# Performance work log

Measured on AMD Instinct MI355X. Metric: run time of the kernel, lower is better.

Reference implementation:

```python
import jax, jax.numpy as jnp
import numpy as np

B, S, D = 4, 1024, 2048
H, G = 16, 2            # num_heads, num_groups (GQA)
HD = D // H             # head_dim = 128


def rotate_half(x):
    x1, x2 = x[..., : x.shape[-1] // 2], x[..., x.shape[-1] // 2 :]
    return jnp.concatenate([-x2, x1], axis=-1)


def setup_inputs() -> dict:
    key = jax.random.key(0)
    ks = jax.random.split(key, 9)
    scale = 0.02
    return {
        "x": jax.random.normal(ks[0], (B, S, D), jnp.float32),
        "wq": jax.random.normal(ks[1], (D, D), jnp.float32) * scale,
        "bq": jnp.zeros((D,), jnp.float32),
        "wk": jax.random.normal(ks[2], (D, G * HD), jnp.float32) * scale,
        "bk": jnp.zeros((G * HD,), jnp.float32),
        "wv": jax.random.normal(ks[3], (D, G * HD), jnp.float32) * scale,
        "bv": jnp.zeros((G * HD,), jnp.float32),
        "wo": jax.random.normal(ks[4], (D, D), jnp.float32) * scale,
        "bo": jnp.zeros((D,), jnp.float32),
    }


def reference(x, wq, bq, wk, bk, wv, bv, wo, bo):
    b, s, d = x.shape
    hd = HD
    # projections (flax Linear: y = x @ kernel + bias)
    q = (x @ wq + bq).reshape(b, s, H, hd)
    k = (x @ wk + bk).reshape(b, s, G, hd)
    v = (x @ wv + bv).reshape(b, s, G, hd)

    # RoPE tables (positions = arange(s), matching q_pos/kv_pos defaults)
    inv_freq = 1.0 / 10000 ** (jnp.arange(0, hd, 2, dtype=jnp.float32) / hd)
    t = jnp.arange(s, dtype=jnp.float32)
    freqs = jnp.outer(t, inv_freq)              # [s, hd/2]
    freqs = jnp.concatenate([freqs, freqs], -1)  # [s, hd]
    sin = jnp.sin(freqs)[:, None, :]             # [s, 1, hd]
    cos = jnp.cos(freqs)[:, None, :]

    q = q * cos + rotate_half(q) * sin
    q = q * (hd ** -0.5)  # module's explicit scale
    k = k * cos + rotate_half(k) * sin

    # GQA: expand K/V groups to full heads (repeats = H // G)
    reps = H // G
    k_exp = jnp.repeat(k, reps, axis=2)  # [b, s, H, hd]
    v_exp = jnp.repeat(v, reps, axis=2)

    # jax.nn.dot_product_attention also applies 1/sqrt(hd) by default,
    # so net scaling is hd**-1 (faithful to the original module).
    scores = jnp.einsum("bqhd,bkhd->bhqk", q, k_exp) * (hd ** -0.5)
    attn = jax.nn.softmax(scores, axis=-1)
    out = jnp.einsum("bhqk,bkhd->bqhd", attn, v_exp).reshape(b, s, d)
    return out @ wo + bo
```

## Files before the change

kernel.cpp:

```cpp
#include <hip/hip_runtime.h>
#include <hip/hip_bf16.h>
#include <type_traits>

typedef __attribute__((ext_vector_type(8))) __bf16 bf16x8;
typedef __attribute__((ext_vector_type(4))) float floatx4;

__device__ inline floatx4 mfma_bf16(bf16x8 a, bf16x8 b, floatx4 c) {
    return __builtin_amdgcn_mfma_f32_16x16x32_bf16(a, b, c, 0, 0, 0);
}

__device__ inline void g2l16(const __hip_bfloat16* g, __hip_bfloat16* l) {
    __builtin_amdgcn_global_load_lds(
        (const __attribute__((address_space(1))) void*)g,
        (__attribute__((address_space(3))) void*)l, 16, 0, 0);
}

__global__ void cast_f32_bf16_k(const float* __restrict__ in,
                                __hip_bfloat16* __restrict__ out, int n4) {
    int i = blockIdx.x * blockDim.x + threadIdx.x;
    if (i < n4) {
        float4 v = ((const float4*)in)[i];
        ushort4 u;
        __hip_bfloat16 a0 = __float2bfloat16(v.x), a1 = __float2bfloat16(v.y);
        __hip_bfloat16 a2 = __float2bfloat16(v.z), a3 = __float2bfloat16(v.w);
        u.x = *(unsigned short*)&a0; u.y = *(unsigned short*)&a1;
        u.z = *(unsigned short*)&a2; u.w = *(unsigned short*)&a3;
        ((ushort4*)out)[i] = u;
    }
}

__global__ void prep_k(const float* __restrict__ wq, const float* __restrict__ wk,
                       const float* __restrict__ wv, const float* __restrict__ wo,
                       const float* __restrict__ bq, const float* __restrict__ bk,
                       const float* __restrict__ bv,
                       __hip_bfloat16* __restrict__ wqkvt,
                       __hip_bfloat16* __restrict__ wot,
                       float* __restrict__ bqkv) {
    int bid = blockIdx.x;
    if (bid >= 9216) {
        int i = (bid - 9216) * 256 + threadIdx.x;
        if (i < 2560)
            bqkv[i] = (i < 2048) ? bq[i] : (i < 2304 ? bk[i - 2048] : bv[i - 2304]);
        return;
    }
    const float* W; __hip_bfloat16* Wt; int C, row_off, cb, rb;
    if (bid < 4096)      { W = wq; Wt = wqkvt; C = 2048; row_off = 0;
                           cb = bid & 63; rb = bid >> 6; }
    else if (bid < 4608) { W = wk; Wt = wqkvt; C = 256;  row_off = 2048;
                           int id = bid - 4096; cb = id & 7; rb = id >> 3; }
    else if (bid < 5120) { W = wv; Wt = wqkvt; C = 256;  row_off = 2304;
                           int id = bid - 4608; cb = id & 7; rb = id >> 3; }
    else                 { W = wo; Wt = wot;   C = 2048; row_off = 0;
                           int id = bid - 5120; cb = id & 63; rb = id >> 6; }
    __shared__ float tile[32][33];
    int c0 = cb * 32, r0 = rb * 32;
    int tx = threadIdx.x & 31, ty0 = threadIdx.x >> 5;
#pragma unroll
    for (int i = 0; i < 4; i++) {
        int ty = ty0 + i * 8;
        tile[ty][tx] = W[(size_t)(r0 + ty) * C + c0 + tx];
    }
    __syncthreads();
#pragma unroll
    for (int i = 0; i < 4; i++) {
        int ty = ty0 + i * 8;
        Wt[(size_t)(row_off + c0 + ty) * 2048 + r0 + tx] = __float2bfloat16(tile[tx][ty]);
    }
}

__global__ __launch_bounds__(256) void gemm_qkv_k(
    const __hip_bfloat16* __restrict__ A,
    const __hip_bfloat16* __restrict__ Bt,
    const float* __restrict__ bias,
    __hip_bfloat16* __restrict__ Qb,
    __hip_bfloat16* __restrict__ Kb,
    __hip_bfloat16* __restrict__ Vlin) {
    __shared__ alignas(16) __hip_bfloat16 As[128 * 32];
    __shared__ alignas(16) __hip_bfloat16 Bs[128 * 32];
    const int t = threadIdx.x, lane = t & 63, w = t >> 6;
    const int quad = lane >> 4, l16 = lane & 15;
    const int bm = blockIdx.y, bn = blockIdx.x;
    const int r_ = t >> 2;
    const int kc_ = (t & 3) ^ ((t >> 3) & 3);
    const int swz = (l16 >> 1) & 3;

    const __hip_bfloat16* gA = A + (size_t)(bm * 128 + r_) * 2048 + kc_ * 8;
    const __hip_bfloat16* gB = Bt + (size_t)(bn * 128 + r_) * 2048 + kc_ * 8;

    floatx4 acc[2][8] = {};

    for (int kt = 0; kt < 2048; kt += 32) {
        g2l16(gA + kt, As + t * 8);
        g2l16(gA + kt + 64 * 2048, As + (t + 256) * 8);
        g2l16(gB + kt, Bs + t * 8);
        g2l16(gB + kt + 64 * 2048, Bs + (t + 256) * 8);
        __syncthreads();
        bf16x8 af[2], bfr[8];
#pragma unroll
        for (int mi = 0; mi < 2; mi++)
            af[mi] = *(const bf16x8*)(As + (w * 32 + mi * 16 + l16) * 32 + (quad ^ swz) * 8);
#pragma unroll
        for (int ni = 0; ni < 8; ni++)
            bfr[ni] = *(const bf16x8*)(Bs + (ni * 16 + l16) * 32 + (quad ^ swz) * 8);
#pragma unroll
        for (int mi = 0; mi < 2; mi++)
#pragma unroll
            for (int ni = 0; ni < 8; ni++)
                acc[mi][ni] = mfma_bf16(af[mi], bfr[ni], acc[mi][ni]);
        __syncthreads();
    }

    const int row_base = bm * 128 + w * 32 + quad * 4;
    if (bn < 18) {
        const float scale = (bn < 16) ? 0.0078125f : 1.0f;
        __hip_bfloat16* dst = (bn < 16) ? Qb : Kb;
        const int nh = (bn < 16) ? 16 : 2;
        const int hh = (bn < 16) ? bn : (bn - 16);
#pragma unroll
        for (int ni = 0; ni < 4; ni++) {
            int j = ni * 16 + l16;
            float invf = __expf(-(float)j * (9.210340371976184f / 64.f));
            float bj  = bias[bn * 128 + j];
            float bj2 = bias[bn * 128 + j + 64];
#pragma unroll
            for (int mi = 0; mi < 2; mi++)
#pragma unroll
                for (int r = 0; r < 4; r++) {
                    int row = row_base + mi * 16 + r;
                    int b = row >> 10, s = row & 1023;
                    float vj  = acc[mi][ni][r] + bj;
                    float vj2 = acc[mi][ni + 4][r] + bj2;
                    float sn, cs;
                    __sincosf((float)s * invf, &sn, &cs);
                    __hip_bfloat16* op = dst + ((size_t)(b * nh + hh) * 1024 + s) * 128;
                    op[j]      = __float2bfloat16((vj * cs - vj2 * sn) * scale);
                    op[j + 64] = __float2bfloat16((vj2 * cs + vj * sn) * scale);
                }
        }
    } else {
        int g = bn - 18;
#pragma unroll
        for (int ni = 0; ni < 8; ni++) {
            int col = ni * 16 + l16;
            float bv = bias[bn * 128 + col];
#pragma unroll
            for (int mi = 0; mi < 2; mi++)
#pragma unroll
                for (int r = 0; r < 4; r++) {
                    int row = row_base + mi * 16 + r;
                    Vlin[(size_t)row * 256 + g * 128 + col] =
                        __float2bfloat16(acc[mi][ni][r] + bv);
                }
        }
    }
}

template <typename OUT_T>
__global__ __launch_bounds__(256) void gemm_bt_k(
    const __hip_bfloat16* __restrict__ A,
    const __hip_bfloat16* __restrict__ Bt,
    const float* __restrict__ bias,
    OUT_T* __restrict__ C,
    int M, int N, int K) {
    __shared__ alignas(16) __hip_bfloat16 As[128 * 32];
    __shared__ alignas(16) __hip_bfloat16 Bs[128 * 32];
    const int t = threadIdx.x;
    const int lane = t & 63;
    const int w = t >> 6;
    const int wm = w & 1, wn = w >> 1;
    const int quad = lane >> 4, l16 = lane & 15;
    const int bm = blockIdx.y, bn = blockIdx.x;
    const int r_ = t >> 2;
    const int kc_ = (t & 3) ^ ((t >> 3) & 3);
    const int swz = (l16 >> 1) & 3;

    const __hip_bfloat16* gA = A + (size_t)(bm * 128 + r_) * K + kc_ * 8;
    const __hip_bfloat16* gB = Bt + (size_t)(bn * 128 + r_) * K + kc_ * 8;

    floatx4 acc[4][4] = {};

    for (int kt = 0; kt < K; kt += 32) {
        g2l16(gA + kt, As + t * 8);
        g2l16(gA + kt + (size_t)64 * K, As + (t + 256) * 8);
        g2l16(gB + kt, Bs + t * 8);
        g2l16(gB + kt + (size_t)64 * K, Bs + (t + 256) * 8);
        __syncthreads();
        bf16x8 af[4], bfr[4];
#pragma unroll
        for (int mi = 0; mi < 4; mi++)
            af[mi] = *(const bf16x8*)(As + (wm * 64 + mi * 16 + l16) * 32 + (quad ^ swz) * 8);
#pragma unroll
        for (int ni = 0; ni < 4; ni++)
            bfr[ni] = *(const bf16x8*)(Bs + (wn * 64 + ni * 16 + l16) * 32 + (quad ^ swz) * 8);
#pragma unroll
        for (int mi = 0; mi < 4; mi++)
#pragma unroll
            for (int ni = 0; ni < 4; ni++)
                acc[mi][ni] = mfma_bf16(af[mi], bfr[ni], acc[mi][ni]);
        __syncthreads();
    }

#pragma unroll
    for (int mi = 0; mi < 4; mi++) {
        int row0 = bm * 128 + wm * 64 + mi * 16 + quad * 4;
#pragma unroll
        for (int ni = 0; ni < 4; ni++) {
            int col = bn * 128 + wn * 64 + ni * 16 + l16;
            float bv = bias[col];
#pragma unroll
            for (int r = 0; r < 4; r++) {
                float v = acc[mi][ni][r] + bv;
                if constexpr (std::is_same<OUT_T, float>::value)
                    C[(size_t)(row0 + r) * N + col] = v;
                else
                    C[(size_t)(row0 + r) * N + col] = __float2bfloat16(v);
            }
        }
    }
}

__global__ void transpose_v_k(const __hip_bfloat16* __restrict__ Vlin,
                              __hip_bfloat16* __restrict__ VT) {
    __shared__ __hip_bfloat16 tile[32][33];
    int bg = blockIdx.z;
    int b = bg >> 1, g = bg & 1;
    int s0 = blockIdx.y * 32, d0 = blockIdx.x * 32;
    int tx = threadIdx.x & 31, ty0 = threadIdx.x >> 5;
#pragma unroll
    for (int i = 0; i < 4; i++) {
        int ty = ty0 + i * 8;
        tile[ty][tx] = Vlin[(size_t)(b * 1024 + s0 + ty) * 256 + g * 128 + d0 + tx];
    }
    __syncthreads();
#pragma unroll
    for (int i = 0; i < 4; i++) {
        int ty = ty0 + i * 8;
        VT[((size_t)(b * 2 + g) * 128 + d0 + ty) * 1024 + s0 + tx] = tile[tx][ty];
    }
}

__global__ __launch_bounds__(256, 2) void attn_k(
    const __hip_bfloat16* __restrict__ Qb,
    const __hip_bfloat16* __restrict__ Kb,
    const __hip_bfloat16* __restrict__ VT,
    __hip_bfloat16* __restrict__ AO) {
    constexpr int PLD = 72;
    __shared__ alignas(16) __hip_bfloat16 Ks[64 * 128];
    __shared__ alignas(16) __hip_bfloat16 Vs[128 * 64];
    __shared__ alignas(16) __hip_bfloat16 Ps[4][32 * PLD];

    const int bh = blockIdx.x;
    const int b = bh >> 4, h = bh & 15, g = h >> 3;
    const int t = threadIdx.x, lane = t & 63, w = t >> 6;
    const int quad = lane >> 4, l16 = lane & 15;
    const int q0 = blockIdx.y * 128 + w * 32;

    const __hip_bfloat16* Qp = Qb + ((size_t)bh * 1024 + q0 + l16) * 128 + quad * 8;
    bf16x8 aq[2][4];
#pragma unroll
    for (int mi = 0; mi < 2; mi++)
#pragma unroll
        for (int kc = 0; kc < 4; kc++)
            aq[mi][kc] = *(const bf16x8*)(Qp + mi * 16 * 128 + kc * 32);

    const int bg = b * 2 + g;
    const __hip_bfloat16* Kstage = Kb + (size_t)bg * 1024 * 128
        + (t >> 4) * 128 + ((t & 15) ^ (t >> 4)) * 8;
    const __hip_bfloat16* Vstage = VT + (size_t)bg * 128 * 1024
        + (t >> 3) * 1024 + ((t & 7) ^ ((t >> 3) & 7)) * 8;

    float l_part[2][4] = {};
    floatx4 o[2][8] = {};

    for (int kv = 0; kv < 1024; kv += 64) {
#pragma unroll
        for (int j = 0; j < 4; j++)
            g2l16(Kstage + (size_t)(kv + j * 16) * 128, Ks + (j * 256 + t) * 8);
#pragma unroll
        for (int j = 0; j < 4; j++)
            g2l16(Vstage + (size_t)j * 32 * 1024 + kv, Vs + (j * 256 + t) * 8);
        __syncthreads();

        floatx4 s[2][4] = {};
#pragma unroll
        for (int nj = 0; nj < 4; nj++)
#pragma unroll
            for (int kc = 0; kc < 4; kc++) {
                bf16x8 kb = *(const bf16x8*)(Ks + (nj * 16 + l16) * 128
                                             + (((kc * 4 + quad) ^ l16) * 8));
                s[0][nj] = mfma_bf16(aq[0][kc], kb, s[0][nj]);
                s[1][nj] = mfma_bf16(aq[1][kc], kb, s[1][nj]);
            }

        __hip_bfloat16* pl = Ps[w];
#pragma unroll
        for (int mi = 0; mi < 2; mi++)
#pragma unroll
            for (int nj = 0; nj < 4; nj++)
#pragma unroll
                for (int r = 0; r < 4; r++) {
                    float p = __expf(s[mi][nj][r]);
                    l_part[mi][r] += p;
                    pl[(mi * 16 + quad * 4 + r) * PLD + nj * 16 + l16] =
                        __float2bfloat16(p);
                }
        asm volatile("s_waitcnt lgkmcnt(0)" ::: "memory");

        bf16x8 ap[2][2];
#pragma unroll
        for (int mi = 0; mi < 2; mi++)
#pragma unroll
            for (int kc2 = 0; kc2 < 2; kc2++)
                ap[mi][kc2] = *(const bf16x8*)(pl + (mi * 16 + l16) * PLD
                                               + kc2 * 32 + quad * 8);

#pragma unroll
        for (int ni = 0; ni < 8; ni++)
#pragma unroll
            for (int kc2 = 0; kc2 < 2; kc2++) {
                bf16x8 vb = *(const bf16x8*)(Vs + (ni * 16 + l16) * 64
                                             + (((kc2 * 4 + quad) ^ (l16 & 7)) * 8));
                o[0][ni] = mfma_bf16(ap[0][kc2], vb, o[0][ni]);
                o[1][ni] = mfma_bf16(ap[1][kc2], vb, o[1][ni]);
            }
        __syncthreads();
    }

#pragma unroll
    for (int mi = 0; mi < 2; mi++)
#pragma unroll
        for (int r = 0; r < 4; r++) {
            float sum = l_part[mi][r];
            sum += __shfl_xor(sum, 1);
            sum += __shfl_xor(sum, 2);
            sum += __shfl_xor(sum, 4);
            sum += __shfl_xor(sum, 8);
            float inv = 1.f / sum;
            size_t srow = (size_t)b * 1024 + q0 + mi * 16 + quad * 4 + r;
#pragma unroll
            for (int ni = 0; ni < 8; ni++)
                AO[srow * 2048 + h * 128 + ni * 16 + l16] =
                    __float2bfloat16(o[mi][ni][r] * inv);
        }
}

extern "C" void kernel_launch(void* const* d_in, const int* in_sizes, int n_in,
                              void* d_out, int out_size, void* d_ws, size_t ws_size,
                              hipStream_t stream) {
    (void)in_sizes; (void)n_in; (void)out_size; (void)ws_size;
    const float* x  = (const float*)d_in[0];
    const float* wq = (const float*)d_in[1];
    const float* bq = (const float*)d_in[2];
    const float* wk = (const float*)d_in[3];
    const float* bk = (const float*)d_in[4];
    const float* wv = (const float*)d_in[5];
    const float* bv = (const float*)d_in[6];
    const float* wo = (const float*)d_in[7];
    const float* bo = (const float*)d_in[8];
    float* out = (float*)d_out;

    char* ws = (char*)d_ws;
    __hip_bfloat16* xb    = (__hip_bfloat16*)(ws + 0);
    __hip_bfloat16* AO    = xb;
    __hip_bfloat16* wqkvt = (__hip_bfloat16*)(ws + 16777216);
    __hip_bfloat16* wot   = (__hip_bfloat16*)(ws + 27262976);
    __hip_bfloat16* Qb    = (__hip_bfloat16*)(ws + 35651584);
    __hip_bfloat16* Kb    = (__hip_bfloat16*)(ws + 52428800);
    __hip_bfloat16* Vlin  = (__hip_bfloat16*)(ws + 54525952);
    __hip_bfloat16* VT    = (__hip_bfloat16*)(ws + 56623104);
    float*          bqkv  = (float*)(ws + 58720256);

    cast_f32_bf16_k<<<8192, 256, 0, stream>>>(x, xb, 2097152);
    prep_k<<<9226, 256, 0, stream>>>(wq, wk, wv, wo, bq, bk, bv, wqkvt, wot, bqkv);
    gemm_qkv_k<<<dim3(20, 32), 256, 0, stream>>>(xb, wqkvt, bqkv, Qb, Kb, Vlin);
    transpose_v_k<<<dim3(4, 32, 8), 256, 0, stream>>>(Vlin, VT);
    attn_k<<<dim3(64, 8), 256, 0, stream>>>(Qb, Kb, VT, AO);
    gemm_bt_k<float><<<dim3(16, 32), 256, 0, stream>>>(AO, wot, bo, out, 4096, 2048, 2048);
}
```

Baseline: 281.4 us.

## Merge cast into prep kernel and double GEMM K-tile to 64 with XOR swizzle

Measured after the change: 287.1 us. +2.0%, slower.

```diff
diff --git a/kernel.cpp b/kernel.cpp
--- a/kernel.cpp
+++ b/kernel.cpp
@@ -15,43 +15,45 @@
         (__attribute__((address_space(3))) void*)l, 16, 0, 0);
 }
 
-__global__ void cast_f32_bf16_k(const float* __restrict__ in,
-                                __hip_bfloat16* __restrict__ out, int n4) {
-    int i = blockIdx.x * blockDim.x + threadIdx.x;
-    if (i < n4) {
-        float4 v = ((const float4*)in)[i];
+__global__ void prep_k(const float* __restrict__ x,
+                       const float* __restrict__ wq, const float* __restrict__ wk,
+                       const float* __restrict__ wv, const float* __restrict__ wo,
+                       const float* __restrict__ bq, const float* __restrict__ bk,
+                       const float* __restrict__ bv,
+                       __hip_bfloat16* __restrict__ xb,
+                       __hip_bfloat16* __restrict__ wqkvt,
+                       __hip_bfloat16* __restrict__ wot,
+                       float* __restrict__ bqkv) {
+    int bid = blockIdx.x;
+    if (bid < 8192) {
+        int i = bid * 256 + threadIdx.x;
+        float4 v = ((const float4*)x)[i];
         ushort4 u;
         __hip_bfloat16 a0 = __float2bfloat16(v.x), a1 = __float2bfloat16(v.y);
         __hip_bfloat16 a2 = __float2bfloat16(v.z), a3 = __float2bfloat16(v.w);
         u.x = *(unsigned short*)&a0; u.y = *(unsigned short*)&a1;
         u.z = *(unsigned short*)&a2; u.w = *(unsigned short*)&a3;
-        ((ushort4*)out)[i] = u;
-    }
-}
-
-__global__ void prep_k(const float* __restrict__ wq, const float* __restrict__ wk,
-                       const float* __restrict__ wv, const float* __restrict__ wo,
-                       const float* __restrict__ bq, const float* __restrict__ bk,
-                       const float* __restrict__ bv,
-                       __hip_bfloat16* __restrict__ wqkvt,
-                       __hip_bfloat16* __restrict__ wot,
-                       float* __restrict__ bqkv) {
-    int bid = blockIdx.x;
-    if (bid >= 9216) {
-        int i = (bid - 9216) * 256 + threadIdx.x;
-        if (i < 2560)
-            bqkv[i] = (i < 2048) ? bq[i] : (i < 2304 ? bk[i - 2048] : bv[i - 2304]);
+        ((ushort4*)xb)[i] = u;
         return;
     }
+    if (bid >= 17408) {
+#pragma unroll
+        for (int it = 0; it < 10; it++) {
+            int i = it * 256 + threadIdx.x;
+            if (i < 2560)
+                bqkv[i] = (i < 2048) ? bq[i] : (i < 2304 ? bk[i - 2048] : bv[i - 2304]);
+        }
+        return;
+    }
     const float* W; __hip_bfloat16* Wt; int C, row_off, cb, rb;
-    if (bid < 4096)      { W = wq; Wt = wqkvt; C = 2048; row_off = 0;
-                           cb = bid & 63; rb = bid >> 6; }
-    else if (bid < 4608) { W = wk; Wt = wqkvt; C = 256;  row_off = 2048;
-                           int id = bid - 4096; cb = id & 7; rb = id >> 3; }
-    else if (bid < 5120) { W = wv; Wt = wqkvt; C = 256;  row_off = 2304;
-                           int id = bid - 4608; cb = id & 7; rb = id >> 3; }
-    else                 { W = wo; Wt = wot;   C = 2048; row_off = 0;
-                           int id = bid - 5120; cb = id & 63; rb = id >> 6; }
+    if (bid < 12288)      { W = wq; Wt = wqkvt; C = 2048; row_off = 0;
+                            int id = bid - 8192;  cb = id & 63; rb = id >> 6; }
+    else if (bid < 12800) { W = wk; Wt = wqkvt; C = 256;  row_off = 2048;
+                            int id = bid - 12288; cb = id & 7;  rb = id >> 3; }
+    else if (bid < 13312) { W = wv; Wt = wqkvt; C = 256;  row_off = 2304;
+                            int id = bid - 12800; cb = id & 7;  rb = id >> 3; }
+    else                  { W = wo; Wt = wot;   C = 2048; row_off = 0;
+                            int id = bid - 13312; cb = id & 63; rb = id >> 6; }
     __shared__ float tile[32][33];
     int c0 = cb * 32, r0 = rb * 32;
     int tx = threadIdx.x & 31, ty0 = threadIdx.x >> 5;
@@ -75,38 +77,42 @@
     __hip_bfloat16* __restrict__ Qb,
     __hip_bfloat16* __restrict__ Kb,
     __hip_bfloat16* __restrict__ Vlin) {
-    __shared__ alignas(16) __hip_bfloat16 As[128 * 32];
-    __shared__ alignas(16) __hip_bfloat16 Bs[128 * 32];
+    __shared__ alignas(16) __hip_bfloat16 As[128 * 64];
+    __shared__ alignas(16) __hip_bfloat16 Bs[128 * 64];
     const int t = threadIdx.x, lane = t & 63, w = t >> 6;
     const int quad = lane >> 4, l16 = lane & 15;
     const int bm = blockIdx.y, bn = blockIdx.x;
-    const int r_ = t >> 2;
-    const int kc_ = (t & 3) ^ ((t >> 3) & 3);
-    const int swz = (l16 >> 1) & 3;
-
-    const __hip_bfloat16* gA = A + (size_t)(bm * 128 + r_) * 2048 + kc_ * 8;
-    const __hip_bfloat16* gB = Bt + (size_t)(bn * 128 + r_) * 2048 + kc_ * 8;
+    const int r_ = t >> 3;
+    const int c_ = (t & 7) ^ (r_ & 7);
+
+    const __hip_bfloat16* gA = A + (size_t)(bm * 128 + r_) * 2048 + c_ * 8;
+    const __hip_bfloat16* gB = Bt + (size_t)(bn * 128 + r_) * 2048 + c_ * 8;
 
     floatx4 acc[2][8] = {};
 
-    for (int kt = 0; kt < 2048; kt += 32) {
-        g2l16(gA + kt, As + t * 8);
-        g2l16(gA + kt + 64 * 2048, As + (t + 256) * 8);
-        g2l16(gB + kt, Bs + t * 8);
-        g2l16(gB + kt + 64 * 2048, Bs + (t + 256) * 8);
-        __syncthreads();
-        bf16x8 af[2], bfr[8];
-#pragma unroll
-        for (int mi = 0; mi < 2; mi++)
-            af[mi] = *(const bf16x8*)(As + (w * 32 + mi * 16 + l16) * 32 + (quad ^ swz) * 8);
-#pragma unroll
-        for (int ni = 0; ni < 8; ni++)
-            bfr[ni] = *(const bf16x8*)(Bs + (ni * 16 + l16) * 32 + (quad ^ swz) * 8);
-#pragma unroll
-        for (int mi = 0; mi < 2; mi++)
+    for (int kt = 0; kt < 2048; kt += 64) {
+#pragma unroll
+        for (int j = 0; j < 4; j++) {
+            g2l16(gA + (size_t)j * 32 * 2048 + kt, As + (j * 256 + t) * 8);
+            g2l16(gB + (size_t)j * 32 * 2048 + kt, Bs + (j * 256 + t) * 8);
+        }
+        __syncthreads();
+#pragma unroll
+        for (int kh = 0; kh < 2; kh++) {
+            const int pc = (((kh << 2) + quad) ^ (l16 & 7)) * 8;
+            bf16x8 af[2], bfr[8];
+#pragma unroll
+            for (int mi = 0; mi < 2; mi++)
+                af[mi] = *(const bf16x8*)(As + (w * 32 + mi * 16 + l16) * 64 + pc);
 #pragma unroll
             for (int ni = 0; ni < 8; ni++)
-                acc[mi][ni] = mfma_bf16(af[mi], bfr[ni], acc[mi][ni]);
+                bfr[ni] = *(const bf16x8*)(Bs + (ni * 16 + l16) * 64 + pc);
+#pragma unroll
+            for (int mi = 0; mi < 2; mi++)
+#pragma unroll
+                for (int ni = 0; ni < 8; ni++)
+                    acc[mi][ni] = mfma_bf16(af[mi], bfr[ni], acc[mi][ni]);
+        }
         __syncthreads();
     }
 
@@ -162,41 +168,43 @@
     const float* __restrict__ bias,
     OUT_T* __restrict__ C,
     int M, int N, int K) {
-    __shared__ alignas(16) __hip_bfloat16 As[128 * 32];
-    __shared__ alignas(16) __hip_bfloat16 Bs[128 * 32];
-    const int t = threadIdx.x;
-    const int lane = t & 63;
-    const int w = t >> 6;
+    __shared__ alignas(16) __hip_bfloat16 As[128 * 64];
+    __shared__ alignas(16) __hip_bfloat16 Bs[128 * 64];
+    const int t = threadIdx.x, lane = t & 63, w = t >> 6;
     const int wm = w & 1, wn = w >> 1;
     const int quad = lane >> 4, l16 = lane & 15;
     const int bm = blockIdx.y, bn = blockIdx.x;
-    const int r_ = t >> 2;
-    const int kc_ = (t & 3) ^ ((t >> 3) & 3);
-    const int swz = (l16 >> 1) & 3;
-
-    const __hip_bfloat16* gA = A + (size_t)(bm * 128 + r_) * K + kc_ * 8;
-    const __hip_bfloat16* gB = Bt + (size_t)(bn * 128 + r_) * K + kc_ * 8;
+    const int r_ = t >> 3;
+    const int c_ = (t & 7) ^ (r_ & 7);
+
+    const __hip_bfloat16* gA = A + (size_t)(bm * 128 + r_) * K + c_ * 8;
+    const __hip_bfloat16* gB = Bt + (size_t)(bn * 128 + r_) * K + c_ * 8;
 
     floatx4 acc[4][4] = {};
 
-    for (int kt = 0; kt < K; kt += 32) {
-        g2l16(gA + kt, As + t * 8);
-        g2l16(gA + kt + (size_t)64 * K, As + (t + 256) * 8);
-        g2l16(gB + kt, Bs + t * 8);
-        g2l16(gB + kt + (size_t)64 * K, Bs + (t + 256) * 8);
-        __syncthreads();
-        bf16x8 af[4], bfr[4];
-#pragma unroll
-        for (int mi = 0; mi < 4; mi++)
-            af[mi] = *(const bf16x8*)(As + (wm * 64 + mi * 16 + l16) * 32 + (quad ^ swz) * 8);
-#pragma unroll
-        for (int ni = 0; ni < 4; ni++)
-            bfr[ni] = *(const bf16x8*)(Bs + (wn * 64 + ni * 16 + l16) * 32 + (quad ^ swz) * 8);
-#pragma unroll
-        for (int mi = 0; mi < 4; mi++)
+    for (int kt = 0; kt < K; kt += 64) {
+#pragma unroll
+        for (int j = 0; j < 4; j++) {
+            g2l16(gA + (size_t)j * 32 * K + kt, As + (j * 256 + t) * 8);
+            g2l16(gB + (size_t)j * 32 * K + kt, Bs + (j * 256 + t) * 8);
+        }
+        __syncthreads();
+#pragma unroll
+        for (int kh = 0; kh < 2; kh++) {
+            const int pc = (((kh << 2) + quad) ^ (l16 & 7)) * 8;
+            bf16x8 af[4], bfr[4];
+#pragma unroll
+            for (int mi = 0; mi < 4; mi++)
+                af[mi] = *(const bf16x8*)(As + (wm * 64 + mi * 16 + l16) * 64 + pc);
 #pragma unroll
             for (int ni = 0; ni < 4; ni++)
-                acc[mi][ni] = mfma_bf16(af[mi], bfr[ni], acc[mi][ni]);
+                bfr[ni] = *(const bf16x8*)(Bs + (wn * 64 + ni * 16 + l16) * 64 + pc);
+#pragma unroll
+            for (int mi = 0; mi < 4; mi++)
+#pragma unroll
+                for (int ni = 0; ni < 4; ni++)
+                    acc[mi][ni] = mfma_bf16(af[mi], bfr[ni], acc[mi][ni]);
+        }
         __syncthreads();
     }
 
@@ -370,8 +378,8 @@
     __hip_bfloat16* VT    = (__hip_bfloat16*)(ws + 56623104);
     float*          bqkv  = (float*)(ws + 58720256);
 
-    cast_f32_bf16_k<<<8192, 256, 0, stream>>>(x, xb, 2097152);
-    prep_k<<<9226, 256, 0, stream>>>(wq, wk, wv, wo, bq, bk, bv, wqkvt, wot, bqkv);
+    prep_k<<<17409, 256, 0, stream>>>(x, wq, wk, wv, wo, bq, bk, bv,
+                                      xb, wqkvt, wot, bqkv);
     gemm_qkv_k<<<dim3(20, 32), 256, 0, stream>>>(xb, wqkvt, bqkv, Qb, Kb, Vlin);
     transpose_v_k<<<dim3(4, 32, 8), 256, 0, stream>>>(Vlin, VT);
     attn_k<<<dim3(64, 8), 256, 0, stream>>>(Qb, Kb, VT, AO);
```

## Merge cast into prep kernel and halve attention rows per wave

Applied to the files above, without the earlier changes.

Measured after the change: 288.8 us. 1.03x slower.

```diff
diff --git a/kernel.cpp b/kernel.cpp
--- a/kernel.cpp
+++ b/kernel.cpp
@@ -15,43 +15,45 @@
         (__attribute__((address_space(3))) void*)l, 16, 0, 0);
 }
 
-__global__ void cast_f32_bf16_k(const float* __restrict__ in,
-                                __hip_bfloat16* __restrict__ out, int n4) {
-    int i = blockIdx.x * blockDim.x + threadIdx.x;
-    if (i < n4) {
-        float4 v = ((const float4*)in)[i];
+__global__ void prep_k(const float* __restrict__ x,
+                       const float* __restrict__ wq, const float* __restrict__ wk,
+                       const float* __restrict__ wv, const float* __restrict__ wo,
+                       const float* __restrict__ bq, const float* __restrict__ bk,
+                       const float* __restrict__ bv,
+                       __hip_bfloat16* __restrict__ xb,
+                       __hip_bfloat16* __restrict__ wqkvt,
+                       __hip_bfloat16* __restrict__ wot,
+                       float* __restrict__ bqkv) {
+    int bid = blockIdx.x;
+    if (bid < 8192) {
+        int i = bid * 256 + threadIdx.x;
+        float4 v = ((const float4*)x)[i];
         ushort4 u;
         __hip_bfloat16 a0 = __float2bfloat16(v.x), a1 = __float2bfloat16(v.y);
         __hip_bfloat16 a2 = __float2bfloat16(v.z), a3 = __float2bfloat16(v.w);
         u.x = *(unsigned short*)&a0; u.y = *(unsigned short*)&a1;
         u.z = *(unsigned short*)&a2; u.w = *(unsigned short*)&a3;
-        ((ushort4*)out)[i] = u;
-    }
-}
-
-__global__ void prep_k(const float* __restrict__ wq, const float* __restrict__ wk,
-                       const float* __restrict__ wv, const float* __restrict__ wo,
-                       const float* __restrict__ bq, const float* __restrict__ bk,
-                       const float* __restrict__ bv,
-                       __hip_bfloat16* __restrict__ wqkvt,
-                       __hip_bfloat16* __restrict__ wot,
-                       float* __restrict__ bqkv) {
-    int bid = blockIdx.x;
-    if (bid >= 9216) {
-        int i = (bid - 9216) * 256 + threadIdx.x;
-        if (i < 2560)
-            bqkv[i] = (i < 2048) ? bq[i] : (i < 2304 ? bk[i - 2048] : bv[i - 2304]);
+        ((ushort4*)xb)[i] = u;
         return;
     }
+    if (bid >= 17408) {
+#pragma unroll
+        for (int it = 0; it < 10; it++) {
+            int i = it * 256 + threadIdx.x;
+            if (i < 2560)
+                bqkv[i] = (i < 2048) ? bq[i] : (i < 2304 ? bk[i - 2048] : bv[i - 2304]);
+        }
+        return;
+    }
     const float* W; __hip_bfloat16* Wt; int C, row_off, cb, rb;
-    if (bid < 4096)      { W = wq; Wt = wqkvt; C = 2048; row_off = 0;
-                           cb = bid & 63; rb = bid >> 6; }
-    else if (bid < 4608) { W = wk; Wt = wqkvt; C = 256;  row_off = 2048;
-                           int id = bid - 4096; cb = id & 7; rb = id >> 3; }
-    else if (bid < 5120) { W = wv; Wt = wqkvt; C = 256;  row_off = 2304;
-                           int id = bid - 4608; cb = id & 7; rb = id >> 3; }
-    else                 { W = wo; Wt = wot;   C = 2048; row_off = 0;
-                           int id = bid - 5120; cb = id & 63; rb = id >> 6; }
+    if (bid < 12288)      { W = wq; Wt = wqkvt; C = 2048; row_off = 0;
+                            int id = bid - 8192;  cb = id & 63; rb = id >> 6; }
+    else if (bid < 12800) { W = wk; Wt = wqkvt; C = 256;  row_off = 2048;
+                            int id = bid - 12288; cb = id & 7;  rb = id >> 3; }
+    else if (bid < 13312) { W = wv; Wt = wqkvt; C = 256;  row_off = 2304;
+                            int id = bid - 12800; cb = id & 7;  rb = id >> 3; }
+    else                  { W = wo; Wt = wot;   C = 2048; row_off = 0;
+                            int id = bid - 13312; cb = id & 63; rb = id >> 6; }
     __shared__ float tile[32][33];
     int c0 = cb * 32, r0 = rb * 32;
     int tx = threadIdx.x & 31, ty0 = threadIdx.x >> 5;
@@ -239,7 +241,7 @@
     }
 }
 
-__global__ __launch_bounds__(256, 2) void attn_k(
+__global__ __launch_bounds__(256, 3) void attn_k(
     const __hip_bfloat16* __restrict__ Qb,
     const __hip_bfloat16* __restrict__ Kb,
     const __hip_bfloat16* __restrict__ VT,
@@ -247,21 +249,19 @@
     constexpr int PLD = 72;
     __shared__ alignas(16) __hip_bfloat16 Ks[64 * 128];
     __shared__ alignas(16) __hip_bfloat16 Vs[128 * 64];
-    __shared__ alignas(16) __hip_bfloat16 Ps[4][32 * PLD];
+    __shared__ alignas(16) __hip_bfloat16 Ps[4][16 * PLD];
 
     const int bh = blockIdx.x;
     const int b = bh >> 4, h = bh & 15, g = h >> 3;
     const int t = threadIdx.x, lane = t & 63, w = t >> 6;
     const int quad = lane >> 4, l16 = lane & 15;
-    const int q0 = blockIdx.y * 128 + w * 32;
+    const int q0 = blockIdx.y * 64 + w * 16;
 
     const __hip_bfloat16* Qp = Qb + ((size_t)bh * 1024 + q0 + l16) * 128 + quad * 8;
-    bf16x8 aq[2][4];
-#pragma unroll
-    for (int mi = 0; mi < 2; mi++)
-#pragma unroll
-        for (int kc = 0; kc < 4; kc++)
-            aq[mi][kc] = *(const bf16x8*)(Qp + mi * 16 * 128 + kc * 32);
+    bf16x8 aq[4];
+#pragma unroll
+    for (int kc = 0; kc < 4; kc++)
+        aq[kc] = *(const bf16x8*)(Qp + kc * 32);
 
     const int bg = b * 2 + g;
     const __hip_bfloat16* Kstage = Kb + (size_t)bg * 1024 * 128
@@ -269,8 +269,8 @@
     const __hip_bfloat16* Vstage = VT + (size_t)bg * 128 * 1024
         + (t >> 3) * 1024 + ((t & 7) ^ ((t >> 3) & 7)) * 8;
 
-    float l_part[2][4] = {};
-    floatx4 o[2][8] = {};
+    float l_part[4] = {};
+    floatx4 o[8] = {};
 
     for (int kv = 0; kv < 1024; kv += 64) {
 #pragma unroll
@@ -281,38 +281,31 @@
             g2l16(Vstage + (size_t)j * 32 * 1024 + kv, Vs + (j * 256 + t) * 8);
         __syncthreads();
 
-        floatx4 s[2][4] = {};
+        floatx4 s[4] = {};
 #pragma unroll
         for (int nj = 0; nj < 4; nj++)
 #pragma unroll
             for (int kc = 0; kc < 4; kc++) {
                 bf16x8 kb = *(const bf16x8*)(Ks + (nj * 16 + l16) * 128
                                              + (((kc * 4 + quad) ^ l16) * 8));
-                s[0][nj] = mfma_bf16(aq[0][kc], kb, s[0][nj]);
-                s[1][nj] = mfma_bf16(aq[1][kc], kb, s[1][nj]);
+                s[nj] = mfma_bf16(aq[kc], kb, s[nj]);
             }
 
         __hip_bfloat16* pl = Ps[w];
 #pragma unroll
-        for (int mi = 0; mi < 2; mi++)
-#pragma unroll
-            for (int nj = 0; nj < 4; nj++)
-#pragma unroll
-                for (int r = 0; r < 4; r++) {
-                    float p = __expf(s[mi][nj][r]);
-                    l_part[mi][r] += p;
-                    pl[(mi * 16 + quad * 4 + r) * PLD + nj * 16 + l16] =
-                        __float2bfloat16(p);
-                }
+        for (int nj = 0; nj < 4; nj++)
+#pragma unroll
+            for (int r = 0; r < 4; r++) {
+                float p = __expf(s[nj][r]);
+                l_part[r] += p;
+                pl[(quad * 4 + r) * PLD + nj * 16 + l16] = __float2bfloat16(p);
+            }
         asm volatile("s_waitcnt lgkmcnt(0)" ::: "memory");
 
-        bf16x8 ap[2][2];
-#pragma unroll
-        for (int mi = 0; mi < 2; mi++)
-#pragma unroll
-            for (int kc2 = 0; kc2 < 2; kc2++)
-                ap[mi][kc2] = *(const bf16x8*)(pl + (mi * 16 + l16) * PLD
-                                               + kc2 * 32 + quad * 8);
+        bf16x8 ap[2];
+#pragma unroll
+        for (int kc2 = 0; kc2 < 2; kc2++)
+            ap[kc2] = *(const bf16x8*)(pl + (size_t)l16 * PLD + kc2 * 32 + quad * 8);
 
 #pragma unroll
         for (int ni = 0; ni < 8; ni++)
@@ -320,28 +313,25 @@
             for (int kc2 = 0; kc2 < 2; kc2++) {
                 bf16x8 vb = *(const bf16x8*)(Vs + (ni * 16 + l16) * 64
                                              + (((kc2 * 4 + quad) ^ (l16 & 7)) * 8));
-                o[0][ni] = mfma_bf16(ap[0][kc2], vb, o[0][ni]);
-                o[1][ni] = mfma_bf16(ap[1][kc2], vb, o[1][ni]);
+                o[ni] = mfma_bf16(ap[kc2], vb, o[ni]);
             }
         __syncthreads();
     }
 
 #pragma unroll
-    for (int mi = 0; mi < 2; mi++)
-#pragma unroll
-        for (int r = 0; r < 4; r++) {
-            float sum = l_part[mi][r];
-            sum += __shfl_xor(sum, 1);
-            sum += __shfl_xor(sum, 2);
-            sum += __shfl_xor(sum, 4);
-            sum += __shfl_xor(sum, 8);
-            float inv = 1.f / sum;
-            size_t srow = (size_t)b * 1024 + q0 + mi * 16 + quad * 4 + r;
-#pragma unroll
-            for (int ni = 0; ni < 8; ni++)
-                AO[srow * 2048 + h * 128 + ni * 16 + l16] =
-                    __float2bfloat16(o[mi][ni][r] * inv);
-        }
+    for (int r = 0; r < 4; r++) {
+        float sum = l_part[r];
+        sum += __shfl_xor(sum, 1);
+        sum += __shfl_xor(sum, 2);
+        sum += __shfl_xor(sum, 4);
+        sum += __shfl_xor(sum, 8);
+        float inv = 1.f / sum;
+        size_t srow = (size_t)b * 1024 + q0 + quad * 4 + r;
+#pragma unroll
+        for (int ni = 0; ni < 8; ni++)
+            AO[srow * 2048 + h * 128 + ni * 16 + l16] =
+                __float2bfloat16(o[ni][r] * inv);
+    }
 }
 
 extern "C" void kernel_launch(void* const* d_in, const int* in_sizes, int n_in,
@@ -370,10 +360,10 @@
     __hip_bfloat16* VT    = (__hip_bfloat16*)(ws + 56623104);
     float*          bqkv  = (float*)(ws + 58720256);
 
-    cast_f32_bf16_k<<<8192, 256, 0, stream>>>(x, xb, 2097152);
-    prep_k<<<9226, 256, 0, stream>>>(wq, wk, wv, wo, bq, bk, bv, wqkvt, wot, bqkv);
+    prep_k<<<17409, 256, 0, stream>>>(x, wq, wk, wv, wo, bq, bk, bv,
+                                      xb, wqkvt, wot, bqkv);
     gemm_qkv_k<<<dim3(20, 32), 256, 0, stream>>>(xb, wqkvt, bqkv, Qb, Kb, Vlin);
     transpose_v_k<<<dim3(4, 32, 8), 256, 0, stream>>>(Vlin, VT);
-    attn_k<<<dim3(64, 8), 256, 0, stream>>>(Qb, Kb, VT, AO);
+    attn_k<<<dim3(64, 16), 256, 0, stream>>>(Qb, Kb, VT, AO);
     gemm_bt_k<float><<<dim3(16, 32), 256, 0, stream>>>(AO, wot, bo, out, 4096, 2048, 2048);
 }
```

## Fuse V transpose into QKV GEMM epilogue and merge cast into prep kernel

Applied to the files above, without the earlier changes.

Result: slower. 299.5 us (+6.5%).

```diff
diff --git a/kernel.cpp b/kernel.cpp
--- a/kernel.cpp
+++ b/kernel.cpp
@@ -15,43 +15,45 @@
         (__attribute__((address_space(3))) void*)l, 16, 0, 0);
 }
 
-__global__ void cast_f32_bf16_k(const float* __restrict__ in,
-                                __hip_bfloat16* __restrict__ out, int n4) {
-    int i = blockIdx.x * blockDim.x + threadIdx.x;
-    if (i < n4) {
-        float4 v = ((const float4*)in)[i];
+__global__ void prep_k(const float* __restrict__ x,
+                       const float* __restrict__ wq, const float* __restrict__ wk,
+                       const float* __restrict__ wv, const float* __restrict__ wo,
+                       const float* __restrict__ bq, const float* __restrict__ bk,
+                       const float* __restrict__ bv,
+                       __hip_bfloat16* __restrict__ xb,
+                       __hip_bfloat16* __restrict__ wqkvt,
+                       __hip_bfloat16* __restrict__ wot,
+                       float* __restrict__ bqkv) {
+    int bid = blockIdx.x;
+    if (bid < 8192) {
+        int i = bid * 256 + threadIdx.x;
+        float4 v = ((const float4*)x)[i];
         ushort4 u;
         __hip_bfloat16 a0 = __float2bfloat16(v.x), a1 = __float2bfloat16(v.y);
         __hip_bfloat16 a2 = __float2bfloat16(v.z), a3 = __float2bfloat16(v.w);
         u.x = *(unsigned short*)&a0; u.y = *(unsigned short*)&a1;
         u.z = *(unsigned short*)&a2; u.w = *(unsigned short*)&a3;
-        ((ushort4*)out)[i] = u;
-    }
-}
-
-__global__ void prep_k(const float* __restrict__ wq, const float* __restrict__ wk,
-                       const float* __restrict__ wv, const float* __restrict__ wo,
-                       const float* __restrict__ bq, const float* __restrict__ bk,
-                       const float* __restrict__ bv,
-                       __hip_bfloat16* __restrict__ wqkvt,
-                       __hip_bfloat16* __restrict__ wot,
-                       float* __restrict__ bqkv) {
-    int bid = blockIdx.x;
-    if (bid >= 9216) {
-        int i = (bid - 9216) * 256 + threadIdx.x;
-        if (i < 2560)
-            bqkv[i] = (i < 2048) ? bq[i] : (i < 2304 ? bk[i - 2048] : bv[i - 2304]);
+        ((ushort4*)xb)[i] = u;
         return;
     }
+    if (bid >= 17408) {
+#pragma unroll
+        for (int it = 0; it < 10; it++) {
+            int i = it * 256 + threadIdx.x;
+            if (i < 2560)
+                bqkv[i] = (i < 2048) ? bq[i] : (i < 2304 ? bk[i - 2048] : bv[i - 2304]);
+        }
+        return;
+    }
     const float* W; __hip_bfloat16* Wt; int C, row_off, cb, rb;
-    if (bid < 4096)      { W = wq; Wt = wqkvt; C = 2048; row_off = 0;
-                           cb = bid & 63; rb = bid >> 6; }
-    else if (bid < 4608) { W = wk; Wt = wqkvt; C = 256;  row_off = 2048;
-                           int id = bid - 4096; cb = id & 7; rb = id >> 3; }
-    else if (bid < 5120) { W = wv; Wt = wqkvt; C = 256;  row_off = 2304;
-                           int id = bid - 4608; cb = id & 7; rb = id >> 3; }
-    else                 { W = wo; Wt = wot;   C = 2048; row_off = 0;
-                           int id = bid - 5120; cb = id & 63; rb = id >> 6; }
+    if (bid < 12288)      { W = wq; Wt = wqkvt; C = 2048; row_off = 0;
+                            int id = bid - 8192;  cb = id & 63; rb = id >> 6; }
+    else if (bid < 12800) { W = wk; Wt = wqkvt; C = 256;  row_off = 2048;
+                            int id = bid - 12288; cb = id & 7;  rb = id >> 3; }
+    else if (bid < 13312) { W = wv; Wt = wqkvt; C = 256;  row_off = 2304;
+                            int id = bid - 12800; cb = id & 7;  rb = id >> 3; }
+    else                  { W = wo; Wt = wot;   C = 2048; row_off = 0;
+                            int id = bid - 13312; cb = id & 63; rb = id >> 6; }
     __shared__ float tile[32][33];
     int c0 = cb * 32, r0 = rb * 32;
     int tx = threadIdx.x & 31, ty0 = threadIdx.x >> 5;
@@ -74,7 +76,7 @@
     const float* __restrict__ bias,
     __hip_bfloat16* __restrict__ Qb,
     __hip_bfloat16* __restrict__ Kb,
-    __hip_bfloat16* __restrict__ Vlin) {
+    __hip_bfloat16* __restrict__ VT) {
     __shared__ alignas(16) __hip_bfloat16 As[128 * 32];
     __shared__ alignas(16) __hip_bfloat16 Bs[128 * 32];
     const int t = threadIdx.x, lane = t & 63, w = t >> 6;
@@ -138,19 +140,33 @@
                 }
         }
     } else {
-        int g = bn - 18;
-#pragma unroll
-        for (int ni = 0; ni < 8; ni++) {
-            int col = ni * 16 + l16;
-            float bv = bias[bn * 128 + col];
+        const int g = bn - 18;
+        const int bg = (bm >> 3) * 2 + g;
+        __hip_bfloat16* tile = ((w < 2) ? As : Bs) + (w & 1) * 2048;
+#pragma unroll
+        for (int p = 0; p < 2; p++) {
 #pragma unroll
             for (int mi = 0; mi < 2; mi++)
 #pragma unroll
-                for (int r = 0; r < 4; r++) {
-                    int row = row_base + mi * 16 + r;
-                    Vlin[(size_t)row * 256 + g * 128 + col] =
-                        __float2bfloat16(acc[mi][ni][r] + bv);
+                for (int nh = 0; nh < 4; nh++) {
+                    int ni = p * 4 + nh;
+                    float bv = bias[bn * 128 + ni * 16 + l16];
+#pragma unroll
+                    for (int r = 0; r < 4; r++)
+                        tile[(mi * 16 + quad * 4 + r) * 64 + nh * 16 + l16] =
+                            __float2bfloat16(acc[mi][ni][r] + bv);
                 }
+            asm volatile("s_waitcnt lgkmcnt(0)" ::: "memory");
+            union { unsigned short us[32]; uint4 q4[4]; } vals;
+#pragma unroll
+            for (int s = 0; s < 32; s++)
+                vals.us[s] = *(const unsigned short*)&tile[s * 64 + lane];
+            asm volatile("s_waitcnt lgkmcnt(0)" ::: "memory");
+            int d = p * 64 + lane;
+            uint4* dst = (uint4*)(VT + ((size_t)(bg * 128 + d)) * 1024
+                                  + (bm & 7) * 128 + w * 32);
+#pragma unroll
+            for (int qi = 0; qi < 4; qi++) dst[qi] = vals.q4[qi];
         }
     }
 }
@@ -219,26 +235,6 @@
     }
 }
 
-__global__ void transpose_v_k(const __hip_bfloat16* __restrict__ Vlin,
-                              __hip_bfloat16* __restrict__ VT) {
-    __shared__ __hip_bfloat16 tile[32][33];
-    int bg = blockIdx.z;
-    int b = bg >> 1, g = bg & 1;
-    int s0 = blockIdx.y * 32, d0 = blockIdx.x * 32;
-    int tx = threadIdx.x & 31, ty0 = threadIdx.x >> 5;
-#pragma unroll
-    for (int i = 0; i < 4; i++) {
-        int ty = ty0 + i * 8;
-        tile[ty][tx] = Vlin[(size_t)(b * 1024 + s0 + ty) * 256 + g * 128 + d0 + tx];
-    }
-    __syncthreads();
-#pragma unroll
-    for (int i = 0; i < 4; i++) {
-        int ty = ty0 + i * 8;
-        VT[((size_t)(b * 2 + g) * 128 + d0 + ty) * 1024 + s0 + tx] = tile[tx][ty];
-    }
-}
-
 __global__ __launch_bounds__(256, 2) void attn_k(
     const __hip_bfloat16* __restrict__ Qb,
     const __hip_bfloat16* __restrict__ Kb,
@@ -366,14 +362,12 @@
     __hip_bfloat16* wot   = (__hip_bfloat16*)(ws + 27262976);
     __hip_bfloat16* Qb    = (__hip_bfloat16*)(ws + 35651584);
     __hip_bfloat16* Kb    = (__hip_bfloat16*)(ws + 52428800);
-    __hip_bfloat16* Vlin  = (__hip_bfloat16*)(ws + 54525952);
     __hip_bfloat16* VT    = (__hip_bfloat16*)(ws + 56623104);
     float*          bqkv  = (float*)(ws + 58720256);
 
-    cast_f32_bf16_k<<<8192, 256, 0, stream>>>(x, xb, 2097152);
-    prep_k<<<9226, 256, 0, stream>>>(wq, wk, wv, wo, bq, bk, bv, wqkvt, wot, bqkv);
-    gemm_qkv_k<<<dim3(20, 32), 256, 0, stream>>>(xb, wqkvt, bqkv, Qb, Kb, Vlin);
-    transpose_v_k<<<dim3(4, 32, 8), 256, 0, stream>>>(Vlin, VT);
+    prep_k<<<17409, 256, 0, stream>>>(x, wq, wk, wv, wo, bq, bk, bv,
+                                      xb, wqkvt, wot, bqkv);
+    gemm_qkv_k<<<dim3(20, 32), 256, 0, stream>>>(xb, wqkvt, bqkv, Qb, Kb, VT);
     attn_k<<<dim3(64, 8), 256, 0, stream>>>(Qb, Kb, VT, AO);
     gemm_bt_k<float><<<dim3(16, 32), 256, 0, stream>>>(AO, wot, bo, out, 4096, 2048, 2048);
 }
```
